# Optimization experiments

Hardware: AMD Instinct MI355X
Metric: run time of the kernel (lower is better)

## Reference

```python
import jax, jax.numpy as jnp
import numpy as np

ALPHA = 2.6
OPTIMAL_RANK = 1.0
SIGMA = 1.8


def setup_inputs() -> dict:
    key = jax.random.key(0)
    k1, k2 = jax.random.split(key)
    B, D, NP = 2048, 768, 8
    q_reps = jax.random.normal(k1, (B, D), dtype=jnp.float32)
    p_reps = jax.random.normal(k2, (B * NP, D), dtype=jnp.float32)
    return {"q_reps": q_reps, "p_reps": p_reps, "n_passages": NP}


def reference(q_reps, p_reps, n_passages):
    B = q_reps.shape[0]
    # [B, P] contrastive score matrix
    scores = jnp.matmul(q_reps, p_reps.T)
    target = jnp.arange(B, dtype=jnp.int32) * n_passages

    # rank position of the positive passage per query (descending argsort)
    rankings = jnp.argsort(-scores, axis=1)            # [B, P]
    positive_rankings = jnp.argmax(
        rankings == target[:, None], axis=1
    ).astype(jnp.float32)                              # [B]

    # per-sample cross-entropy (reduction='none')
    logp = jax.nn.log_softmax(scores, axis=1)
    raw_loss = -jnp.take_along_axis(logp, target[:, None], axis=1)[:, 0]

    # Gaussian rank weighting: w = 1 + alpha * exp(-(r - r_opt)^2 / (2 sigma^2))
    extra_weight = jnp.exp(-((positive_rankings - OPTIMAL_RANK) ** 2) / (2.0 * SIGMA ** 2))
    weights = 1.0 + ALPHA * extra_weight

    loss = jnp.mean(raw_loss * weights)
    return loss
```

## Files before the change

kernel.cpp:

```cpp
#include <hip/hip_runtime.h>
#include <math.h>


#define BQ 2048
#define DD 768
#define NPASS 8
#define PP 16384
#define BM 256
#define BN 256
#define BK 64
#define KITERS 12
#define NBLK 64
#define MBLK 8
#define NCHUNKS 256

#define ALPHA_C 2.6f
#define INV_2SIG2 (1.0f/6.48f)

typedef __attribute__((ext_vector_type(4))) float floatx4;
typedef __attribute__((ext_vector_type(2))) long longx2;

#define NQ16   98304
#define NTOT16 884736
#define NCB16  3456
__global__ __launch_bounds__(256) void prep_kernel(const float* __restrict__ qf,
                                                   const float* __restrict__ pf,
                                                   uint4* __restrict__ qb,
                                                   uint4* __restrict__ pb,
                                                   float* __restrict__ st,
                                                   float* __restrict__ out) {
  const int b = blockIdx.x;
  if (b == 0 && threadIdx.x == 0) *out = 0.f;
  if (b < NCB16) {
    const int i = b * 256 + threadIdx.x;
    const float4* src; uint4* dst;
    if (i < NQ16) { src = (const float4*)qf + 4 * (size_t)i; dst = qb + i; }
    else { const size_t j = (size_t)i - NQ16; src = (const float4*)pf + 4 * j; dst = pb + j; }
    const float4 v0 = src[0], v1 = src[1], v2 = src[2], v3 = src[3];
    unsigned u0 = __builtin_amdgcn_cvt_pk_fp8_f32(v0.x, v0.y, 0, 0);
    u0 = __builtin_amdgcn_cvt_pk_fp8_f32(v0.z, v0.w, u0, 1);
    unsigned u1 = __builtin_amdgcn_cvt_pk_fp8_f32(v1.x, v1.y, 0, 0);
    u1 = __builtin_amdgcn_cvt_pk_fp8_f32(v1.z, v1.w, u1, 1);
    unsigned u2 = __builtin_amdgcn_cvt_pk_fp8_f32(v2.x, v2.y, 0, 0);
    u2 = __builtin_amdgcn_cvt_pk_fp8_f32(v2.z, v2.w, u2, 1);
    unsigned u3 = __builtin_amdgcn_cvt_pk_fp8_f32(v3.x, v3.y, 0, 0);
    u3 = __builtin_amdgcn_cvt_pk_fp8_f32(v3.z, v3.w, u3, 1);
    uint4 w; w.x = u0; w.y = u1; w.z = u2; w.w = u3;
    *dst = w;
  } else {
    const int wv = threadIdx.x >> 6, lane = threadIdx.x & 63;
    const int qi = (b - NCB16) * 4 + wv;
    const float4* q4 = (const float4*)(qf + (size_t)qi * DD);
    const float4* p4 = (const float4*)(pf + (size_t)qi * NPASS * DD);
    float acc = 0.f;
#pragma unroll
    for (int u = 0; u < 3; ++u) {
      float4 a = q4[lane + 64 * u];
      float4 c = p4[lane + 64 * u];
      acc = fmaf(a.x, c.x, acc);
      acc = fmaf(a.y, c.y, acc);
      acc = fmaf(a.z, c.z, acc);
      acc = fmaf(a.w, c.w, acc);
    }
#pragma unroll
    for (int off = 32; off >= 1; off >>= 1) acc += __shfl_xor(acc, off);
    if (lane == 0) st[qi] = acc;
  }
}

__global__ __launch_bounds__(1024) void gemm_kernel(const unsigned char* __restrict__ qb,
                                                    const unsigned char* __restrict__ pb,
                                                    const float* __restrict__ st,
                                                    float* __restrict__ pm,
                                                    float* __restrict__ pl,
                                                    float* __restrict__ pc) {
  __shared__ unsigned char As[3][16 * 1024];
  __shared__ unsigned char Bs[3][16 * 1024];
  __shared__ float st_lds[BM];

  const int t = threadIdx.x;
  const int lane = t & 63;
  const int wv = t >> 6;
  const int wm = wv >> 2, wn = wv & 3;
  const int bid = blockIdx.x;
  const int xcd = bid & 7;
  const int nb = xcd * 8 + ((bid >> 3) & 7);
  const int mb = bid >> 6;
  const int qbase = mb * BM;
  const int n0 = nb * BN;
  const int lm = lane & 15;
  const int lq = lane >> 4;
  const int lds_lane = lane * 16;

  if (t < BM) st_lds[t] = st[qbase + t];

  floatx4 acc[4][4];
#pragma unroll
  for (int i = 0; i < 4; ++i)
#pragma unroll
    for (int j = 0; j < 4; ++j) acc[i][j] = (floatx4){0.f, 0.f, 0.f, 0.f};

  const size_t arow = (size_t)(qbase + wv * 16 + lm) * DD;
  const size_t brow = (size_t)(n0 + wv * 16 + lm) * DD;
  const int intra16 = lq * 256 + lm * 16;

#define STAGE(KT, BUF)                                                          \
  {                                                                             \
    const size_t koff = (size_t)(KT) * BK + lq * 16;                            \
    __builtin_amdgcn_global_load_lds(                                           \
        (const __attribute__((address_space(1))) void*)(qb + arow + koff),      \
        (__attribute__((address_space(3))) void*)(&As[BUF][wv * 1024] + lds_lane), \
        16, 0, 0);                                                              \
    __builtin_amdgcn_global_load_lds(                                           \
        (const __attribute__((address_space(1))) void*)(pb + brow + koff),      \
        (__attribute__((address_space(3))) void*)(&Bs[BUF][wv * 1024] + lds_lane), \
        16, 0, 0);                                                              \
  }

#define MFMA8(II, JJ)                                                           \
  {                                                                             \
    acc[II][JJ]       = __builtin_amdgcn_mfma_f32_16x16x32_fp8_fp8(a2[II].x,     b2[JJ].x,     acc[II][JJ],       0, 0, 0); \
    acc[II][JJ+1]     = __builtin_amdgcn_mfma_f32_16x16x32_fp8_fp8(a2[II].x,     b2[JJ+1].x,   acc[II][JJ+1],     0, 0, 0); \
    acc[II+1][JJ]     = __builtin_amdgcn_mfma_f32_16x16x32_fp8_fp8(a2[II+1].x,   b2[JJ].x,     acc[II+1][JJ],     0, 0, 0); \
    acc[II+1][JJ+1]   = __builtin_amdgcn_mfma_f32_16x16x32_fp8_fp8(a2[II+1].x,   b2[JJ+1].x,   acc[II+1][JJ+1],   0, 0, 0); \
    acc[II][JJ]       = __builtin_amdgcn_mfma_f32_16x16x32_fp8_fp8(a2[II].y,     b2[JJ].y,     acc[II][JJ],       0, 0, 0); \
    acc[II][JJ+1]     = __builtin_amdgcn_mfma_f32_16x16x32_fp8_fp8(a2[II].y,     b2[JJ+1].y,   acc[II][JJ+1],     0, 0, 0); \
    acc[II+1][JJ]     = __builtin_amdgcn_mfma_f32_16x16x32_fp8_fp8(a2[II+1].y,   b2[JJ].y,     acc[II+1][JJ],     0, 0, 0); \
    acc[II+1][JJ+1]   = __builtin_amdgcn_mfma_f32_16x16x32_fp8_fp8(a2[II+1].y,   b2[JJ+1].y,   acc[II+1][JJ+1],   0, 0, 0); \
  }

#define COMPUTE(CB)                                                             \
  {                                                                             \
    longx2 a2[4], b2[4];                                                        \
    a2[0] = *(const longx2*)(&As[CB][(wm * 4 + 0) * 1024] + intra16);           \
    a2[1] = *(const longx2*)(&As[CB][(wm * 4 + 1) * 1024] + intra16);           \
    b2[0] = *(const longx2*)(&Bs[CB][(wn * 4 + 0) * 1024] + intra16);           \
    b2[1] = *(const longx2*)(&Bs[CB][(wn * 4 + 1) * 1024] + intra16);           \
    __builtin_amdgcn_sched_barrier(0);                                          \
    b2[2] = *(const longx2*)(&Bs[CB][(wn * 4 + 2) * 1024] + intra16);           \
    b2[3] = *(const longx2*)(&Bs[CB][(wn * 4 + 3) * 1024] + intra16);           \
    __builtin_amdgcn_sched_barrier(0);                                          \
    __builtin_amdgcn_s_setprio(1);                                              \
    MFMA8(0, 0)                                                                 \
    __builtin_amdgcn_s_setprio(0);                                              \
    __builtin_amdgcn_sched_barrier(0);                                          \
    a2[2] = *(const longx2*)(&As[CB][(wm * 4 + 2) * 1024] + intra16);           \
    a2[3] = *(const longx2*)(&As[CB][(wm * 4 + 3) * 1024] + intra16);           \
    __builtin_amdgcn_sched_barrier(0);                                          \
    __builtin_amdgcn_s_setprio(1);                                              \
    MFMA8(0, 2)                                                                 \
    __builtin_amdgcn_s_setprio(0);                                              \
    __builtin_amdgcn_sched_barrier(0);                                          \
    __builtin_amdgcn_s_setprio(1);                                              \
    MFMA8(2, 0)                                                                 \
    MFMA8(2, 2)                                                                 \
    __builtin_amdgcn_s_setprio(0);                                              \
  }

  STAGE(0, 0)
  STAGE(1, 1)
  int cur = 0;
  int stg = 2;
  for (int kt = 0; kt < KITERS - 1; ++kt) {
    asm volatile("s_waitcnt vmcnt(2)" ::: "memory");
    __builtin_amdgcn_s_barrier();
    __builtin_amdgcn_sched_barrier(0);
    if (kt < KITERS - 2) STAGE(kt + 2, stg)
    COMPUTE(cur)
    cur = (cur == 2) ? 0 : cur + 1;
    stg = (stg == 2) ? 0 : stg + 1;
  }
  asm volatile("s_waitcnt vmcnt(0)" ::: "memory");
  __builtin_amdgcn_s_barrier();
  __builtin_amdgcn_sched_barrier(0);
  COMPUTE(cur)

  const int chunk = nb * 4 + wn;
  float* const pmc = pm + (size_t)chunk * BQ;
  float* const plc = pl + (size_t)chunk * BQ;
  float* const pcc = pc + (size_t)chunk * BQ;
#pragma unroll
  for (int i = 0; i < 4; ++i) {
#pragma unroll
    for (int r = 0; r < 4; ++r) {
      const int rl = wm * 64 + i * 16 + lq * 4 + r;
      float mx = fmaxf(fmaxf(acc[i][0][r], acc[i][1][r]),
                       fmaxf(acc[i][2][r], acc[i][3][r]));
#pragma unroll
      for (int off = 1; off <= 8; off <<= 1) mx = fmaxf(mx, __shfl_xor(mx, off));
      const float stv = st_lds[rl];
      const int qg = qbase + rl;
      const int tcol = qg * NPASS;
      float sum = 0.f, c = 0.f;
#pragma unroll
      for (int j = 0; j < 4; ++j) {
        const float s = acc[i][j][r];
        sum += __expf(s - mx);
        const int cg = n0 + wn * 64 + j * 16 + lm;
        if (s > stv && cg != tcol) c += 1.f;
      }
#pragma unroll
      for (int off = 1; off <= 8; off <<= 1) {
        sum += __shfl_xor(sum, off);
        c += __shfl_xor(c, off);
      }
      if (lm == 0) {
        pmc[qg] = mx; plc[qg] = sum; pcc[qg] = c;
      }
    }
  }
}

__global__ __launch_bounds__(256) void merge_kernel(const float* __restrict__ pm,
                                                    const float* __restrict__ pl,
                                                    const float* __restrict__ pc,
                                                    float* __restrict__ pm2,
                                                    float* __restrict__ pl2,
                                                    float* __restrict__ pc2) {
  const int wv = threadIdx.x >> 6, lane = threadIdx.x & 63;
  const int q = (blockIdx.x & 31) * 64 + lane;
  const int slice = blockIdx.x >> 5;
  const int c0 = slice * 32 + wv * 8;
  float m = -1e30f, l = 0.f, c = 0.f;
#pragma unroll
  for (int ch = 0; ch < 8; ++ch) {
    const size_t idx = (size_t)(c0 + ch) * BQ + q;
    const float mv = pm[idx], lv = pl[idx], cv = pc[idx];
    const float nm = fmaxf(m, mv);
    l = l * __expf(m - nm) + lv * __expf(mv - nm);
    m = nm; c += cv;
  }
  __shared__ float sm[4][64], sl[4][64], sc[4][64];
  sm[wv][lane] = m; sl[wv][lane] = l; sc[wv][lane] = c;
  __syncthreads();
  if (wv == 0) {
    float M = sm[0][lane], L = sl[0][lane], C = sc[0][lane];
#pragma unroll
    for (int w = 1; w < 4; ++w) {
      const float mv = sm[w][lane];
      const float nm = fmaxf(M, mv);
      L = L * __expf(M - nm) + sl[w][lane] * __expf(mv - nm);
      M = nm; C += sc[w][lane];
    }
    const size_t o = (size_t)slice * BQ + q;
    pm2[o] = M; pl2[o] = L; pc2[o] = C;
  }
}

__global__ __launch_bounds__(64) void finalize_kernel(const float* __restrict__ st,
                                                      const float* __restrict__ pm2,
                                                      const float* __restrict__ pl2,
                                                      const float* __restrict__ pc2,
                                                      float* __restrict__ out) {
  const int lane = threadIdx.x;
  const int q = blockIdx.x * 64 + lane;
  float m = -1e30f, l = 0.f, c = 0.f;
#pragma unroll
  for (int s = 0; s < 8; ++s) {
    const size_t idx = (size_t)s * BQ + q;
    const float mv = pm2[idx], lv = pl2[idx], cv = pc2[idx];
    const float nm = fmaxf(m, mv);
    l = l * __expf(m - nm) + lv * __expf(mv - nm);
    m = nm; c += cv;
  }
  const float raw = logf(l) + m - st[q];
  const float dr = c - 1.0f;
  const float w = 1.0f + ALPHA_C * __expf(-(dr * dr) * INV_2SIG2);
  float loss = raw * w * (1.0f / (float)BQ);
#pragma unroll
  for (int off = 32; off >= 1; off >>= 1) loss += __shfl_xor(loss, off);
  if (lane == 0) atomicAdd(out, loss);
}

extern "C" void kernel_launch(void* const* d_in, const int* in_sizes, int n_in,
                              void* d_out, int out_size, void* d_ws, size_t ws_size,
                              hipStream_t stream) {
  const float* q = (const float*)d_in[0];
  const float* p = (const float*)d_in[1];
  char* ws = (char*)d_ws;
  unsigned char* qb = (unsigned char*)ws;
  unsigned char* pb = (unsigned char*)(ws + 1572864);
  float* st = (float*)(ws + 14155776);
  float* pm = (float*)(ws + 14163968);
  float* pl = (float*)(ws + 16261120);
  float* pc = (float*)(ws + 18358272);
  float* pm2 = (float*)(ws + 20455424);
  float* pl2 = (float*)(ws + 20520960);
  float* pc2 = (float*)(ws + 20586496);
  float* out = (float*)d_out;

  prep_kernel<<<NCB16 + BQ / 4, 256, 0, stream>>>(q, p, (uint4*)qb, (uint4*)pb, st, out);
  gemm_kernel<<<NBLK * MBLK, 1024, 0, stream>>>(qb, pb, st, pm, pl, pc);
  merge_kernel<<<256, 256, 0, stream>>>(pm, pl, pc, pm2, pl2, pc2);
  finalize_kernel<<<BQ / 64, 64, 0, stream>>>(st, pm2, pl2, pc2, out);
}
```

Baseline: 146.9 us.

## Switch GEMM to 32x32x64 scaled FP8 MFMA with new LDS layout

Replaces the 16x16x32 fp8 MFMA sequence with the gfx950 scaled 32x32x64 f8f6f4 MFMA, using unit scales, so each wave issues four larger MFMAs per K-step instead of thirty-two small ones. The LDS staging layout changes accordingly: waves 0-7 load A tiles and waves 8-15 load B tiles in 32-row units, and operand fragments are assembled from two 16-byte LDS reads. The epilogue is rewritten for the 32x32 accumulator layout, with reductions across 32 lanes. This aims to cut instruction issue and LDS read overhead, at the cost of a different bank-access pattern and the removal of the hand-tuned interleaving of LDS reads with MFMAs.

Result: slower. 344.7 us (+134.7%).

```diff
diff --git a/kernel.cpp b/kernel.cpp
--- a/kernel.cpp
+++ b/kernel.cpp
@@ -17,8 +17,9 @@
 #define ALPHA_C 2.6f
 #define INV_2SIG2 (1.0f/6.48f)
 
-typedef __attribute__((ext_vector_type(4))) float floatx4;
-typedef __attribute__((ext_vector_type(2))) long longx2;
+typedef __attribute__((ext_vector_type(16))) float floatx16;
+typedef __attribute__((ext_vector_type(4))) int intx4;
+typedef __attribute__((ext_vector_type(8))) int intx8;
 
 #define NQ16   98304
 #define NTOT16 884736
@@ -68,14 +69,14 @@
   }
 }
 
-__global__ __launch_bounds__(1024) void gemm_kernel(const unsigned char* __restrict__ qb,
-                                                    const unsigned char* __restrict__ pb,
-                                                    const float* __restrict__ st,
-                                                    float* __restrict__ pm,
-                                                    float* __restrict__ pl,
-                                                    float* __restrict__ pc) {
-  __shared__ unsigned char As[3][16 * 1024];
-  __shared__ unsigned char Bs[3][16 * 1024];
+__global__ __launch_bounds__(1024, 1) void gemm_kernel(const unsigned char* __restrict__ qb,
+                                                       const unsigned char* __restrict__ pb,
+                                                       const float* __restrict__ st,
+                                                       float* __restrict__ pm,
+                                                       float* __restrict__ pl,
+                                                       float* __restrict__ pc) {
+  __shared__ unsigned char As[3][8 * 2048];
+  __shared__ unsigned char Bs[3][8 * 2048];
   __shared__ float st_lds[BM];
 
   const int t = threadIdx.x;
@@ -88,72 +89,57 @@
   const int mb = bid >> 6;
   const int qbase = mb * BM;
   const int n0 = nb * BN;
-  const int lm = lane & 15;
-  const int lq = lane >> 4;
-  const int lds_lane = lane * 16;
+  const int lm32 = lane & 31;
+  const int lhi = lane >> 5;
 
   if (t < BM) st_lds[t] = st[qbase + t];
 
-  floatx4 acc[4][4];
-#pragma unroll
-  for (int i = 0; i < 4; ++i)
-#pragma unroll
-    for (int j = 0; j < 4; ++j) acc[i][j] = (floatx4){0.f, 0.f, 0.f, 0.f};
-
-  const size_t arow = (size_t)(qbase + wv * 16 + lm) * DD;
-  const size_t brow = (size_t)(n0 + wv * 16 + lm) * DD;
-  const int intra16 = lq * 256 + lm * 16;
+  floatx16 acc[2][2];
+#pragma unroll
+  for (int i = 0; i < 2; ++i)
+#pragma unroll
+    for (int j = 0; j < 2; ++j)
+#pragma unroll
+      for (int r = 0; r < 16; ++r) acc[i][j][r] = 0.f;
+
+  const int srow = (wv < 8) ? (qbase + wv * 32) : (n0 + (wv - 8) * 32);
+  const unsigned char* const sbase =
+      ((wv < 8) ? qb : pb) + (size_t)(srow + lm32) * DD;
 
 #define STAGE(KT, BUF)                                                          \
   {                                                                             \
-    const size_t koff = (size_t)(KT) * BK + lq * 16;                            \
-    __builtin_amdgcn_global_load_lds(                                           \
-        (const __attribute__((address_space(1))) void*)(qb + arow + koff),      \
-        (__attribute__((address_space(3))) void*)(&As[BUF][wv * 1024] + lds_lane), \
-        16, 0, 0);                                                              \
-    __builtin_amdgcn_global_load_lds(                                           \
-        (const __attribute__((address_space(1))) void*)(pb + brow + koff),      \
-        (__attribute__((address_space(3))) void*)(&Bs[BUF][wv * 1024] + lds_lane), \
-        16, 0, 0);                                                              \
-  }
-
-#define MFMA8(II, JJ)                                                           \
+    __attribute__((address_space(3))) unsigned char* ldst =                     \
+        (__attribute__((address_space(3))) unsigned char*)                      \
+        ((wv < 8) ? &As[BUF][wv * 2048] : &Bs[BUF][(wv - 8) * 2048]);           \
+    _Pragma("unroll")                                                           \
+    for (int v = 0; v < 2; ++v) {                                               \
+      __builtin_amdgcn_global_load_lds(                                         \
+          (const __attribute__((address_space(1))) void*)(sbase + (size_t)(KT) * BK + (2 * v + lhi) * 16), \
+          (__attribute__((address_space(3))) void*)(ldst + v * 1024 + lane * 16), \
+          16, 0, 0);                                                            \
+    }                                                                           \
+  }
+
+#define FRAG(dst, ARR, CBUF, UNIT)                                              \
   {                                                                             \
-    acc[II][JJ]       = __builtin_amdgcn_mfma_f32_16x16x32_fp8_fp8(a2[II].x,     b2[JJ].x,     acc[II][JJ],       0, 0, 0); \
-    acc[II][JJ+1]     = __builtin_amdgcn_mfma_f32_16x16x32_fp8_fp8(a2[II].x,     b2[JJ+1].x,   acc[II][JJ+1],     0, 0, 0); \
-    acc[II+1][JJ]     = __builtin_amdgcn_mfma_f32_16x16x32_fp8_fp8(a2[II+1].x,   b2[JJ].x,     acc[II+1][JJ],     0, 0, 0); \
-    acc[II+1][JJ+1]   = __builtin_amdgcn_mfma_f32_16x16x32_fp8_fp8(a2[II+1].x,   b2[JJ+1].x,   acc[II+1][JJ+1],   0, 0, 0); \
-    acc[II][JJ]       = __builtin_amdgcn_mfma_f32_16x16x32_fp8_fp8(a2[II].y,     b2[JJ].y,     acc[II][JJ],       0, 0, 0); \
-    acc[II][JJ+1]     = __builtin_amdgcn_mfma_f32_16x16x32_fp8_fp8(a2[II].y,     b2[JJ+1].y,   acc[II][JJ+1],     0, 0, 0); \
-    acc[II+1][JJ]     = __builtin_amdgcn_mfma_f32_16x16x32_fp8_fp8(a2[II+1].y,   b2[JJ].y,     acc[II+1][JJ],     0, 0, 0); \
-    acc[II+1][JJ+1]   = __builtin_amdgcn_mfma_f32_16x16x32_fp8_fp8(a2[II+1].y,   b2[JJ+1].y,   acc[II+1][JJ+1],   0, 0, 0); \
+    const unsigned char* ub = &ARR[CBUF][(UNIT) * 2048] + lhi * 1024 + lm32 * 16; \
+    intx4 lo = *(const intx4*)ub;                                               \
+    intx4 hi = *(const intx4*)(ub + 512);                                       \
+    dst = __builtin_shufflevector(lo, hi, 0, 1, 2, 3, 4, 5, 6, 7);              \
   }
 
 #define COMPUTE(CB)                                                             \
   {                                                                             \
-    longx2 a2[4], b2[4];                                                        \
-    a2[0] = *(const longx2*)(&As[CB][(wm * 4 + 0) * 1024] + intra16);           \
-    a2[1] = *(const longx2*)(&As[CB][(wm * 4 + 1) * 1024] + intra16);           \
-    b2[0] = *(const longx2*)(&Bs[CB][(wn * 4 + 0) * 1024] + intra16);           \
-    b2[1] = *(const longx2*)(&Bs[CB][(wn * 4 + 1) * 1024] + intra16);           \
-    __builtin_amdgcn_sched_barrier(0);                                          \
-    b2[2] = *(const longx2*)(&Bs[CB][(wn * 4 + 2) * 1024] + intra16);           \
-    b2[3] = *(const longx2*)(&Bs[CB][(wn * 4 + 3) * 1024] + intra16);           \
-    __builtin_amdgcn_sched_barrier(0);                                          \
+    intx8 af[2], bf[2];                                                         \
+    FRAG(af[0], As, CB, wm * 2 + 0)                                             \
+    FRAG(af[1], As, CB, wm * 2 + 1)                                             \
+    FRAG(bf[0], Bs, CB, wn * 2 + 0)                                             \
+    FRAG(bf[1], Bs, CB, wn * 2 + 1)                                             \
     __builtin_amdgcn_s_setprio(1);                                              \
-    MFMA8(0, 0)                                                                 \
-    __builtin_amdgcn_s_setprio(0);                                              \
-    __builtin_amdgcn_sched_barrier(0);                                          \
-    a2[2] = *(const longx2*)(&As[CB][(wm * 4 + 2) * 1024] + intra16);           \
-    a2[3] = *(const longx2*)(&As[CB][(wm * 4 + 3) * 1024] + intra16);           \
-    __builtin_amdgcn_sched_barrier(0);                                          \
-    __builtin_amdgcn_s_setprio(1);                                              \
-    MFMA8(0, 2)                                                                 \
-    __builtin_amdgcn_s_setprio(0);                                              \
-    __builtin_amdgcn_sched_barrier(0);                                          \
-    __builtin_amdgcn_s_setprio(1);                                              \
-    MFMA8(2, 0)                                                                 \
-    MFMA8(2, 2)                                                                 \
+    acc[0][0] = __builtin_amdgcn_mfma_scale_f32_32x32x64_f8f6f4(af[0], bf[0], acc[0][0], 0, 0, 0, 127, 0, 127); \
+    acc[0][1] = __builtin_amdgcn_mfma_scale_f32_32x32x64_f8f6f4(af[0], bf[1], acc[0][1], 0, 0, 0, 127, 0, 127); \
+    acc[1][0] = __builtin_amdgcn_mfma_scale_f32_32x32x64_f8f6f4(af[1], bf[0], acc[1][0], 0, 0, 0, 127, 0, 127); \
+    acc[1][1] = __builtin_amdgcn_mfma_scale_f32_32x32x64_f8f6f4(af[1], bf[1], acc[1][1], 0, 0, 0, 127, 0, 127); \
     __builtin_amdgcn_s_setprio(0);                                              \
   }
 
@@ -179,32 +165,29 @@
   float* const pmc = pm + (size_t)chunk * BQ;
   float* const plc = pl + (size_t)chunk * BQ;
   float* const pcc = pc + (size_t)chunk * BQ;
-#pragma unroll
-  for (int i = 0; i < 4; ++i) {
-#pragma unroll
-    for (int r = 0; r < 4; ++r) {
-      const int rl = wm * 64 + i * 16 + lq * 4 + r;
-      float mx = fmaxf(fmaxf(acc[i][0][r], acc[i][1][r]),
-                       fmaxf(acc[i][2][r], acc[i][3][r]));
-#pragma unroll
-      for (int off = 1; off <= 8; off <<= 1) mx = fmaxf(mx, __shfl_xor(mx, off));
+  const int cgbase = n0 + wn * 64 + lm32;
+#pragma unroll
+  for (int i = 0; i < 2; ++i) {
+#pragma unroll
+    for (int r = 0; r < 16; ++r) {
+      const int rl = wm * 64 + i * 32 + (r & 3) + 8 * (r >> 2) + 4 * lhi;
+      const float s0 = acc[i][0][r], s1 = acc[i][1][r];
+      float mx = fmaxf(s0, s1);
+#pragma unroll
+      for (int off = 1; off <= 16; off <<= 1) mx = fmaxf(mx, __shfl_xor(mx, off));
       const float stv = st_lds[rl];
       const int qg = qbase + rl;
       const int tcol = qg * NPASS;
-      float sum = 0.f, c = 0.f;
-#pragma unroll
-      for (int j = 0; j < 4; ++j) {
-        const float s = acc[i][j][r];
-        sum += __expf(s - mx);
-        const int cg = n0 + wn * 64 + j * 16 + lm;
-        if (s > stv && cg != tcol) c += 1.f;
-      }
-#pragma unroll
-      for (int off = 1; off <= 8; off <<= 1) {
+      float sum = __expf(s0 - mx) + __expf(s1 - mx);
+      float c = 0.f;
+      if (s0 > stv && cgbase != tcol) c += 1.f;
+      if (s1 > stv && cgbase + 32 != tcol) c += 1.f;
+#pragma unroll
+      for (int off = 1; off <= 16; off <<= 1) {
         sum += __shfl_xor(sum, off);
         c += __shfl_xor(c, off);
       }
-      if (lm == 0) {
+      if (lm32 == 0) {
         pmc[qg] = mx; plc[qg] = sum; pcc[qg] = c;
       }
     }
```

## Fuse fp8 conversion of passages into GEMM B-tile staging

Applied to the files above, without the earlier changes.

The prep kernel now converts only the query matrix to fp8. The GEMM loads fp32 passage rows straight from global memory, converts them to fp8 in registers and writes them to LDS. This removes the separate pass that wrote and re-read a 12.6 MB fp8 copy of the passages. In exchange, the GEMM now reads fp32 data, four times the bytes per B tile, and since each passage tile is read by 8 M-blocks, global traffic for B rises. Staging also becomes synchronous register loads, so the waitcnt scheme changes.

Result: slower. 182.3 us (+24.1%).

```diff
diff --git a/kernel.cpp b/kernel.cpp
--- a/kernel.cpp
+++ b/kernel.cpp
@@ -20,22 +20,17 @@
 typedef __attribute__((ext_vector_type(4))) float floatx4;
 typedef __attribute__((ext_vector_type(2))) long longx2;
 
-#define NQ16   98304
-#define NTOT16 884736
-#define NCB16  3456
+#define QCB 384
 __global__ __launch_bounds__(256) void prep_kernel(const float* __restrict__ qf,
                                                    const float* __restrict__ pf,
                                                    uint4* __restrict__ qb,
-                                                   uint4* __restrict__ pb,
                                                    float* __restrict__ st,
                                                    float* __restrict__ out) {
   const int b = blockIdx.x;
   if (b == 0 && threadIdx.x == 0) *out = 0.f;
-  if (b < NCB16) {
+  if (b < QCB) {
     const int i = b * 256 + threadIdx.x;
-    const float4* src; uint4* dst;
-    if (i < NQ16) { src = (const float4*)qf + 4 * (size_t)i; dst = qb + i; }
-    else { const size_t j = (size_t)i - NQ16; src = (const float4*)pf + 4 * j; dst = pb + j; }
+    const float4* src = (const float4*)qf + 4 * (size_t)i;
     const float4 v0 = src[0], v1 = src[1], v2 = src[2], v3 = src[3];
     unsigned u0 = __builtin_amdgcn_cvt_pk_fp8_f32(v0.x, v0.y, 0, 0);
     u0 = __builtin_amdgcn_cvt_pk_fp8_f32(v0.z, v0.w, u0, 1);
@@ -46,10 +41,10 @@
     unsigned u3 = __builtin_amdgcn_cvt_pk_fp8_f32(v3.x, v3.y, 0, 0);
     u3 = __builtin_amdgcn_cvt_pk_fp8_f32(v3.z, v3.w, u3, 1);
     uint4 w; w.x = u0; w.y = u1; w.z = u2; w.w = u3;
-    *dst = w;
+    qb[i] = w;
   } else {
     const int wv = threadIdx.x >> 6, lane = threadIdx.x & 63;
-    const int qi = (b - NCB16) * 4 + wv;
+    const int qi = (b - QCB) * 4 + wv;
     const float4* q4 = (const float4*)(qf + (size_t)qi * DD);
     const float4* p4 = (const float4*)(pf + (size_t)qi * NPASS * DD);
     float acc = 0.f;
@@ -69,7 +64,7 @@
 }
 
 __global__ __launch_bounds__(1024) void gemm_kernel(const unsigned char* __restrict__ qb,
-                                                    const unsigned char* __restrict__ pb,
+                                                    const float* __restrict__ pf,
                                                     const float* __restrict__ st,
                                                     float* __restrict__ pm,
                                                     float* __restrict__ pl,
@@ -101,20 +96,31 @@
     for (int j = 0; j < 4; ++j) acc[i][j] = (floatx4){0.f, 0.f, 0.f, 0.f};
 
   const size_t arow = (size_t)(qbase + wv * 16 + lm) * DD;
-  const size_t brow = (size_t)(n0 + wv * 16 + lm) * DD;
+  const float* const brow = pf + (size_t)(n0 + wv * 16 + lm) * DD;
   const int intra16 = lq * 256 + lm * 16;
 
 #define STAGE(KT, BUF)                                                          \
   {                                                                             \
-    const size_t koff = (size_t)(KT) * BK + lq * 16;                            \
+    const float4* bsrc = (const float4*)(brow + (size_t)(KT) * BK + lq * 16);   \
+    const float4 f0 = bsrc[0], f1 = bsrc[1];                                    \
     __builtin_amdgcn_global_load_lds(                                           \
-        (const __attribute__((address_space(1))) void*)(qb + arow + koff),      \
+        (const __attribute__((address_space(1))) void*)(qb + arow + (size_t)(KT) * BK + lq * 16), \
         (__attribute__((address_space(3))) void*)(&As[BUF][wv * 1024] + lds_lane), \
         16, 0, 0);                                                              \
-    __builtin_amdgcn_global_load_lds(                                           \
-        (const __attribute__((address_space(1))) void*)(pb + brow + koff),      \
-        (__attribute__((address_space(3))) void*)(&Bs[BUF][wv * 1024] + lds_lane), \
-        16, 0, 0);                                                              \
+    unsigned u0 = __builtin_amdgcn_cvt_pk_fp8_f32(f0.x, f0.y, 0, 0);            \
+    u0 = __builtin_amdgcn_cvt_pk_fp8_f32(f0.z, f0.w, u0, 1);                    \
+    unsigned u1 = __builtin_amdgcn_cvt_pk_fp8_f32(f1.x, f1.y, 0, 0);            \
+    u1 = __builtin_amdgcn_cvt_pk_fp8_f32(f1.z, f1.w, u1, 1);                    \
+    uint2 w0; w0.x = u0; w0.y = u1;                                             \
+    *reinterpret_cast<uint2*>(&Bs[BUF][wv * 1024] + lds_lane) = w0;             \
+    __builtin_amdgcn_sched_barrier(0);                                          \
+    const float4 f2 = bsrc[2], f3 = bsrc[3];                                    \
+    unsigned u2 = __builtin_amdgcn_cvt_pk_fp8_f32(f2.x, f2.y, 0, 0);            \
+    u2 = __builtin_amdgcn_cvt_pk_fp8_f32(f2.z, f2.w, u2, 1);                    \
+    unsigned u3 = __builtin_amdgcn_cvt_pk_fp8_f32(f3.x, f3.y, 0, 0);            \
+    u3 = __builtin_amdgcn_cvt_pk_fp8_f32(f3.z, f3.w, u3, 1);                    \
+    uint2 w1; w1.x = u2; w1.y = u3;                                             \
+    *reinterpret_cast<uint2*>(&Bs[BUF][wv * 1024] + lds_lane + 8) = w1;         \
   }
 
 #define MFMA8(II, JJ)                                                           \
@@ -162,7 +168,7 @@
   int cur = 0;
   int stg = 2;
   for (int kt = 0; kt < KITERS - 1; ++kt) {
-    asm volatile("s_waitcnt vmcnt(2)" ::: "memory");
+    asm volatile("s_waitcnt vmcnt(1) lgkmcnt(0)" ::: "memory");
     __builtin_amdgcn_s_barrier();
     __builtin_amdgcn_sched_barrier(0);
     if (kt < KITERS - 2) STAGE(kt + 2, stg)
@@ -170,7 +176,7 @@
     cur = (cur == 2) ? 0 : cur + 1;
     stg = (stg == 2) ? 0 : stg + 1;
   }
-  asm volatile("s_waitcnt vmcnt(0)" ::: "memory");
+  asm volatile("s_waitcnt vmcnt(0) lgkmcnt(0)" ::: "memory");
   __builtin_amdgcn_s_barrier();
   __builtin_amdgcn_sched_barrier(0);
   COMPUTE(cur)
@@ -279,7 +285,6 @@
   const float* p = (const float*)d_in[1];
   char* ws = (char*)d_ws;
   unsigned char* qb = (unsigned char*)ws;
-  unsigned char* pb = (unsigned char*)(ws + 1572864);
   float* st = (float*)(ws + 14155776);
   float* pm = (float*)(ws + 14163968);
   float* pl = (float*)(ws + 16261120);
@@ -289,8 +294,8 @@
   float* pc2 = (float*)(ws + 20586496);
   float* out = (float*)d_out;
 
-  prep_kernel<<<NCB16 + BQ / 4, 256, 0, stream>>>(q, p, (uint4*)qb, (uint4*)pb, st, out);
-  gemm_kernel<<<NBLK * MBLK, 1024, 0, stream>>>(qb, pb, st, pm, pl, pc);
+  prep_kernel<<<QCB + BQ / 4, 256, 0, stream>>>(q, p, (uint4*)qb, st, out);
+  gemm_kernel<<<NBLK * MBLK, 1024, 0, stream>>>(qb, p, st, pm, pl, pc);
   merge_kernel<<<256, 256, 0, stream>>>(pm, pl, pc, pm2, pl2, pc2);
   finalize_kernel<<<BQ / 64, 64, 0, stream>>>(st, pm2, pl2, pc2, out);
 }
```
